# Kernel tuning notes

Hardware: AMD Instinct MI355X
Metric: run time of the kernel (lower is better)

Reference implementation:

```python
import jax, jax.numpy as jnp
import numpy as np

B = 32
HIDDEN = 1152
SEQ_LEN = 4096
FREQ_DIM = 256
MAX_PERIOD = 10000.0


def setup_inputs() -> dict:
    key = jax.random.key(0)
    k_t, k_w1, k_w2 = jax.random.split(key, 3)
    t = jax.random.uniform(k_t, (B,), dtype=jnp.float32, minval=0.0, maxval=1000.0)
    W1 = jax.random.normal(k_w1, (HIDDEN, FREQ_DIM), dtype=jnp.float32) * 0.02
    b1 = jnp.zeros((HIDDEN,), dtype=jnp.float32)
    W2 = jax.random.normal(k_w2, (HIDDEN, HIDDEN), dtype=jnp.float32) * 0.02
    b2 = jnp.zeros((HIDDEN,), dtype=jnp.float32)
    return {"t": t, "W1": W1, "b1": b1, "W2": W2, "b2": b2}


def timestep_embedding(t, dim):
    half = dim // 2
    freqs = jnp.exp(-jnp.log(MAX_PERIOD) * jnp.arange(half, dtype=jnp.float32) / half)
    args = t[:, None] * freqs[None, :]          # [B, half]
    return jnp.concatenate([jnp.cos(args), jnp.sin(args)], axis=-1)  # [B, dim]


def reference(t, W1, b1, W2, b2):
    # [B, FREQ_DIM] sinusoidal embedding
    emb = timestep_embedding(t, FREQ_DIM)
    # 1x1 convs over channel dim are pointwise matmuls; values are identical
    # across the expanded seq dim, so compute once per batch and broadcast.
    h = jax.nn.gelu(jnp.einsum('bf,hf->bh', emb, W1) + b1, approximate=True)
    out = jnp.einsum('bh,oh->bo', h, W2) + b2   # [B, HIDDEN]
    # match original output layout [B, HIDDEN, 1, SEQ_LEN]
    return jnp.broadcast_to(out[:, :, None, None], (B, HIDDEN, 1, SEQ_LEN))
```

## Files before the change

### kernel.cpp

```cpp
#include <hip/hip_runtime.h>
#include <math.h>

#define BATCH   32
#define HIDDEN  1152
#define FREQ    256
#define HALF    128
#define SEQLEN  4096

typedef float vf4 __attribute__((ext_vector_type(4)));

__global__ __launch_bounds__(256) void k_hidden(const float* __restrict__ t,
                                                const float* __restrict__ W1,
                                                const float* __restrict__ b1,
                                                float* __restrict__ h_out) {
    __shared__ float emb[FREQ];
    const int b   = blockIdx.x;
    const int tid = threadIdx.x;
    const float tb = t[b];

    {
        const int   j    = tid & (HALF - 1);
        const float freq = exp2f(-13.287712379549449f * (float)j * (1.0f / (float)HALF));
        const float arg  = tb * freq;
        emb[tid] = (tid < HALF) ? cosf(arg) : sinf(arg);
    }
    __syncthreads();

    for (int o = tid; o < HIDDEN; o += 256) {
        const float4* __restrict__ w4 = reinterpret_cast<const float4*>(W1 + (size_t)o * FREQ);
        float s0 = 0.f, s1 = 0.f, s2 = 0.f, s3 = 0.f;
#pragma unroll 8
        for (int k4 = 0; k4 < FREQ / 4; ++k4) {
            const float4 w = w4[k4];
            s0 += w.x * emb[4 * k4 + 0];
            s1 += w.y * emb[4 * k4 + 1];
            s2 += w.z * emb[4 * k4 + 2];
            s3 += w.w * emb[4 * k4 + 3];
        }
        const float x  = (s0 + s1) + (s2 + s3) + b1[o];
        const float x3 = x * x * x;
        const float g  = 0.5f * x * (1.0f + tanhf(0.7978845608028654f * (x + 0.044715f * x3)));
        h_out[b * HIDDEN + o] = g;
    }
}

__global__ __launch_bounds__(128) void k_out(const float* __restrict__ h,
                                             const float* __restrict__ W2,
                                             const float* __restrict__ b2,
                                             float* __restrict__ outv) {
    __shared__ float hs[HIDDEN];
    const int b = blockIdx.y;
    const int o = blockIdx.x * 128 + threadIdx.x;

    for (int k = threadIdx.x; k < HIDDEN; k += 128)
        hs[k] = h[b * HIDDEN + k];
    __syncthreads();

    const float4* __restrict__ w4 = reinterpret_cast<const float4*>(W2 + (size_t)o * HIDDEN);
    float s0 = 0.f, s1 = 0.f, s2 = 0.f, s3 = 0.f;
#pragma unroll 4
    for (int k4 = 0; k4 < HIDDEN / 4; ++k4) {
        const float4 w = w4[k4];
        s0 += w.x * hs[4 * k4 + 0];
        s1 += w.y * hs[4 * k4 + 1];
        s2 += w.z * hs[4 * k4 + 2];
        s3 += w.w * hs[4 * k4 + 3];
    }
    outv[b * HIDDEN + o] = (s0 + s1) + (s2 + s3) + b2[o];
}

__global__ __launch_bounds__(256) void k_bcast(const float* __restrict__ outv,
                                               vf4* __restrict__ dst) {
    const int gwave  = (blockIdx.x * 256 + threadIdx.x) >> 6;
    const int lane   = threadIdx.x & 63;
    const int nwaves = (gridDim.x * 256) >> 6;
    const int ROWS   = BATCH * HIDDEN;

    for (int row = gwave; row < ROWS; row += nwaves) {
        const float v = outv[row];
        const vf4 val = {v, v, v, v};
        vf4* p = dst + (size_t)row * (SEQLEN / 4) + lane;
#pragma unroll
        for (int it = 0; it < (SEQLEN / 4) / 64; ++it)
            __builtin_nontemporal_store(val, p + it * 64);
    }
}

extern "C" void kernel_launch(void* const* d_in, const int* in_sizes, int n_in,
                              void* d_out, int out_size, void* d_ws, size_t ws_size,
                              hipStream_t stream) {
    const float* t  = (const float*)d_in[0];
    const float* W1 = (const float*)d_in[1];
    const float* b1 = (const float*)d_in[2];
    const float* W2 = (const float*)d_in[3];
    const float* b2 = (const float*)d_in[4];
    float* outf = (float*)d_out;

    float* h  = (float*)d_ws;
    float* ov = h + BATCH * HIDDEN;

    k_hidden<<<BATCH, 256, 0, stream>>>(t, W1, b1, h);
    k_out<<<dim3(HIDDEN / 128, BATCH), 128, 0, stream>>>(h, W2, b2, ov);
    k_bcast<<<2048, 256, 0, stream>>>(ov, (vf4*)outf);
}
```

Before: 685.3 us.

## Fuse MLP kernels and restructure broadcast with regular vectorized stores

Merges the hidden-layer and output-layer kernels into one kernel, where each block recomputes the sinusoidal embedding and GELU hidden vector in shared memory, then splits the W2 dot product across two thread halves. The broadcast kernel now assigns four rows per wave with a single vector load and uses ordinary stores instead of nontemporal stores. This removes one launch and the intermediate global buffer, at the cost of redundant first-layer compute per block and a different store cache policy for the large output write.

```diff
diff --git a/kernel.cpp b/kernel.cpp
--- a/kernel.cpp
+++ b/kernel.cpp
@@ -9,13 +9,19 @@
 
 typedef float vf4 __attribute__((ext_vector_type(4)));
 
-__global__ __launch_bounds__(256) void k_hidden(const float* __restrict__ t,
-                                                const float* __restrict__ W1,
-                                                const float* __restrict__ b1,
-                                                float* __restrict__ h_out) {
+__global__ __launch_bounds__(256) void k_mlp(const float* __restrict__ t,
+                                             const float* __restrict__ W1,
+                                             const float* __restrict__ b1,
+                                             const float* __restrict__ W2,
+                                             const float* __restrict__ b2,
+                                             float* __restrict__ outv) {
     __shared__ float emb[FREQ];
-    const int b   = blockIdx.x;
+    __shared__ float hs[HIDDEN];
+    __shared__ float part[256];
+
     const int tid = threadIdx.x;
+    const int b   = blockIdx.y;
+    const int c   = blockIdx.x;
     const float tb = t[b];
 
     {
@@ -39,50 +45,48 @@
         }
         const float x  = (s0 + s1) + (s2 + s3) + b1[o];
         const float x3 = x * x * x;
-        const float g  = 0.5f * x * (1.0f + tanhf(0.7978845608028654f * (x + 0.044715f * x3)));
-        h_out[b * HIDDEN + o] = g;
+        hs[o] = 0.5f * x * (1.0f + tanhf(0.7978845608028654f * (x + 0.044715f * x3)));
     }
-}
-
-__global__ __launch_bounds__(128) void k_out(const float* __restrict__ h,
-                                             const float* __restrict__ W2,
-                                             const float* __restrict__ b2,
-                                             float* __restrict__ outv) {
-    __shared__ float hs[HIDDEN];
-    const int b = blockIdx.y;
-    const int o = blockIdx.x * 128 + threadIdx.x;
-
-    for (int k = threadIdx.x; k < HIDDEN; k += 128)
-        hs[k] = h[b * HIDDEN + k];
     __syncthreads();
 
-    const float4* __restrict__ w4 = reinterpret_cast<const float4*>(W2 + (size_t)o * HIDDEN);
-    float s0 = 0.f, s1 = 0.f, s2 = 0.f, s3 = 0.f;
+    {
+        const int o    = c * 128 + (tid & 127);
+        const int half = tid >> 7;
+        const int k0   = half * (HIDDEN / 2);
+        const float4* __restrict__ w4 =
+            reinterpret_cast<const float4*>(W2 + (size_t)o * HIDDEN + k0);
+        float s0 = 0.f, s1 = 0.f, s2 = 0.f, s3 = 0.f;
 #pragma unroll 4
-    for (int k4 = 0; k4 < HIDDEN / 4; ++k4) {
-        const float4 w = w4[k4];
-        s0 += w.x * hs[4 * k4 + 0];
-        s1 += w.y * hs[4 * k4 + 1];
-        s2 += w.z * hs[4 * k4 + 2];
-        s3 += w.w * hs[4 * k4 + 3];
+        for (int k4 = 0; k4 < (HIDDEN / 2) / 4; ++k4) {
+            const float4 w = w4[k4];
+            s0 += w.x * hs[k0 + 4 * k4 + 0];
+            s1 += w.y * hs[k0 + 4 * k4 + 1];
+            s2 += w.z * hs[k0 + 4 * k4 + 2];
+            s3 += w.w * hs[k0 + 4 * k4 + 3];
+        }
+        part[tid] = (s0 + s1) + (s2 + s3);
+        __syncthreads();
+        if (tid < 128)
+            outv[b * HIDDEN + o] = part[tid] + part[tid + 128] + b2[o];
     }
-    outv[b * HIDDEN + o] = (s0 + s1) + (s2 + s3) + b2[o];
 }
 
 __global__ __launch_bounds__(256) void k_bcast(const float* __restrict__ outv,
                                                vf4* __restrict__ dst) {
-    const int gwave  = (blockIdx.x * 256 + threadIdx.x) >> 6;
-    const int lane   = threadIdx.x & 63;
-    const int nwaves = (gridDim.x * 256) >> 6;
-    const int ROWS   = BATCH * HIDDEN;
+    const int gwave = (blockIdx.x * 256 + threadIdx.x) >> 6;
+    const int lane  = threadIdx.x & 63;
 
-    for (int row = gwave; row < ROWS; row += nwaves) {
-        const float v = outv[row];
+    const vf4 vals = *reinterpret_cast<const vf4*>(outv + 4 * gwave);
+    vf4* p = dst + (size_t)(4 * gwave) * (SEQLEN / 4) + lane;
+
+#pragma unroll
+    for (int r = 0; r < 4; ++r) {
+        const float v = vals[r];
         const vf4 val = {v, v, v, v};
-        vf4* p = dst + (size_t)row * (SEQLEN / 4) + lane;
+        vf4* q = p + r * (SEQLEN / 4);
 #pragma unroll
         for (int it = 0; it < (SEQLEN / 4) / 64; ++it)
-            __builtin_nontemporal_store(val, p + it * 64);
+            q[it * 64] = val;
     }
 }
 
@@ -96,10 +100,8 @@
     const float* b2 = (const float*)d_in[4];
     float* outf = (float*)d_out;
 
-    float* h  = (float*)d_ws;
-    float* ov = h + BATCH * HIDDEN;
+    float* ov = (float*)d_ws;
 
-    k_hidden<<<BATCH, 256, 0, stream>>>(t, W1, b1, h);
-    k_out<<<dim3(HIDDEN / 128, BATCH), 128, 0, stream>>>(h, W2, b2, ov);
-    k_bcast<<<2048, 256, 0, stream>>>(ov, (vf4*)outf);
+    k_mlp<<<dim3(HIDDEN / 128, BATCH), 256, 0, stream>>>(t, W1, b1, W2, b2, ov);
+    k_bcast<<<(BATCH * HIDDEN) / 16, 256, 0, stream>>>(ov, (vf4*)outf);
 }
```

Measured after the change: 694.5 us. No clear change (+1.3%).
